# Optimization experiments

Measured on AMD Instinct MI355X. Metric: run time of the kernel, lower is better.

The kernel has to match this reference:

```python
import jax, jax.numpy as jnp
import numpy as np

B, C, H, W = 8, 64, 64, 64


def setup_inputs() -> dict:
    key = jax.random.key(0)
    ks = jax.random.split(key, 8)
    s = 1.0 / np.sqrt(C)  # keep logits in a reasonable range
    return {
        "x": jax.random.normal(ks[0], (B, C, H, W), dtype=jnp.float32),
        "Wf": jax.random.normal(ks[1], (C, C), dtype=jnp.float32) * s,
        "bf": jax.random.normal(ks[2], (C,), dtype=jnp.float32) * s,
        "Wg": jax.random.normal(ks[3], (C, C), dtype=jnp.float32) * s,
        "bg": jax.random.normal(ks[4], (C,), dtype=jnp.float32) * s,
        "Wh": jax.random.normal(ks[5], (C, C), dtype=jnp.float32) * s,
        "bh": jax.random.normal(ks[6], (C,), dtype=jnp.float32) * s,
        "gamma": jax.random.normal(ks[7], (1,), dtype=jnp.float32),
    }


def reference(x, Wf, bf, Wg, bg, Wh, bh, gamma):
    b, c, h, w = x.shape
    n = h * w
    xf = x.reshape(b, c, n)  # [B, C, N]
    # 1x1 convs == per-pixel channel GEMMs
    f = jnp.einsum("oc,bcn->bon", Wf, xf) + bf[None, :, None]  # [B, C, N]
    g = jnp.einsum("oc,bcn->bon", Wg, xf) + bg[None, :, None]
    hh = jnp.einsum("oc,bcn->bon", Wh, xf) + bh[None, :, None]
    # att_in[b, i, j] = f[b, :, i] . g[b, :, j]  (f_x permuted then bmm with g_x)
    att = jax.nn.softmax(jnp.einsum("bci,bcj->bij", f, g), axis=-1)  # [B, N, N]
    # torch.bmm(h_x, attention): out[b, c, j] = sum_i h[b, c, i] * att[b, i, j]
    out = jnp.einsum("bci,bij->bcj", hh, att).reshape(b, c, h, w)
    return gamma[0] * out + x
```

## Files before the change

kernel.cpp:

```cpp
#include <hip/hip_runtime.h>

#define BB 8
#define CC 64
#define NN 4096
#define JCH 8
#define LOG2E 1.4426950408889634f

typedef float f32x4  __attribute__((ext_vector_type(4)));
typedef float f32x16 __attribute__((ext_vector_type(16)));
typedef _Float16 half8_t __attribute__((ext_vector_type(8)));
typedef int int4v __attribute__((ext_vector_type(4)));
typedef unsigned uint2v __attribute__((ext_vector_type(2)));


__global__ __launch_bounds__(384, 6) void qkv_kernel(
    const float* __restrict__ x,
    const float* __restrict__ Wf, const float* __restrict__ bf,
    const float* __restrict__ Wg, const float* __restrict__ bg,
    const float* __restrict__ Wh, const float* __restrict__ bh,
    _Float16* __restrict__ fT, _Float16* __restrict__ gT,
    _Float16* __restrict__ hT)
{
    __shared__ float xbuf[64][36];

    const int tid  = threadIdx.x;
    const int lane = tid & 63;
    const int wv   = tid >> 6;
    const int l31  = lane & 31;
    const int q5   = lane >> 5;
    const int z    = wv >> 1;
    const int ot   = wv & 1;
    const int n0   = blockIdx.x * 32;
    const int b    = blockIdx.y;

    if (tid < 256) {
        const int row = tid >> 2;
        const int px4 = (tid & 3) * 8;
        const float* src = x + (size_t)(b * CC + row) * NN + n0 + px4;
        *(f32x4*)&xbuf[row][px4]     = *(const f32x4*)(src);
        *(f32x4*)&xbuf[row][px4 + 4] = *(const f32x4*)(src + 4);
    }
    __syncthreads();

    half8_t xf[4];
#pragma unroll
    for (int kc = 0; kc < 4; ++kc) {
        const int kb = kc * 16 + q5 * 8;
        int4v p;
#pragma unroll
        for (int h2 = 0; h2 < 4; ++h2) {
            p[h2] = __builtin_bit_cast(int, __builtin_amdgcn_cvt_pkrtz(
                xbuf[kb + h2 * 2][l31], xbuf[kb + h2 * 2 + 1][l31]));
        }
        xf[kc] = __builtin_bit_cast(half8_t, p);
    }

    const float* W    = (z == 0) ? Wf : ((z == 1) ? Wg : Wh);
    const float* bias = (z == 0) ? bf : ((z == 1) ? bg : bh);

    half8_t wf[4];
    {
        const float* wrow = W + (size_t)(ot * 32 + l31) * CC;
#pragma unroll
        for (int kc = 0; kc < 4; ++kc) {
            const f32x4 w0 = *(const f32x4*)(wrow + kc * 16 + q5 * 8);
            const f32x4 w1 = *(const f32x4*)(wrow + kc * 16 + q5 * 8 + 4);
            int4v p;
            p[0] = __builtin_bit_cast(int, __builtin_amdgcn_cvt_pkrtz(w0[0], w0[1]));
            p[1] = __builtin_bit_cast(int, __builtin_amdgcn_cvt_pkrtz(w0[2], w0[3]));
            p[2] = __builtin_bit_cast(int, __builtin_amdgcn_cvt_pkrtz(w1[0], w1[1]));
            p[3] = __builtin_bit_cast(int, __builtin_amdgcn_cvt_pkrtz(w1[2], w1[3]));
            wf[kc] = __builtin_bit_cast(half8_t, p);
        }
    }

    if (z < 2) {
        f32x16 acc = {};
#pragma unroll
        for (int kc = 0; kc < 4; ++kc)
            acc = __builtin_amdgcn_mfma_f32_32x32x16_f16(xf[kc], wf[kc], acc, 0, 0, 0);
        _Float16* dstT = (z == 0) ? fT : gT;
        const float scale = (z == 0) ? LOG2E : 1.0f;
        const float bv = bias[ot * 32 + l31];
#pragma unroll
        for (int r = 0; r < 16; ++r) {
            const int prow = (r & 3) + 8 * (r >> 2) + 4 * q5;
            dstT[(size_t)(b * NN + n0 + prow) * CC + ot * 32 + l31] =
                (_Float16)((acc[r] + bv) * scale);
        }
    } else {
        f32x16 acc = {};
#pragma unroll
        for (int kc = 0; kc < 4; ++kc)
            acc = __builtin_amdgcn_mfma_f32_32x32x16_f16(wf[kc], xf[kc], acc, 0, 0, 0);
        _Float16* hbase = hT + ((size_t)(b * (NN / 32) + blockIdx.x) * CC) * 32;
#pragma unroll
        for (int rb = 0; rb < 4; ++rb) {
            const f32x4 b4 = *(const f32x4*)(bias + ot * 32 + rb * 8 + q5 * 4);
#pragma unroll
            for (int k = 0; k < 4; ++k) {
                const int c = ot * 32 + rb * 8 + q5 * 4 + k;
                hbase[(size_t)c * 32 + l31] = (_Float16)(acc[rb * 4 + k] + b4[k]);
            }
        }
    }
}

__global__ __launch_bounds__(256, 4) void stats_kernel(
    const _Float16* __restrict__ fT, const _Float16* __restrict__ gT,
    float* __restrict__ lpart)
{
    __shared__ _Float16 gbuf[2][64][72];

    const int lane = threadIdx.x & 63;
    const int wv   = threadIdx.x >> 6;
    const int b    = blockIdx.y;
    const int jc   = blockIdx.z;
    const int i0   = blockIdx.x * 128 + wv * 32;
    const int l31  = lane & 31;
    const int q5   = lane >> 5;

    half8_t a[4];
    const _Float16* fa = fT + (size_t)(b * NN + i0 + l31) * CC + q5 * 8;
#pragma unroll
    for (int kc = 0; kc < 4; ++kc) a[kc] = *(const half8_t*)(fa + kc * 16);

    const _Float16* gchunk = gT + (size_t)(b * NN + jc * (NN / JCH)) * CC;
    const int T = NN / JCH / 64;

    const int srow = wv * 16 + (lane >> 3);
    const int scol = (lane & 7) * 8;

    {
        const half8_t v0 = *(const half8_t*)(gchunk + (size_t)srow * CC + scol);
        const half8_t v1 = *(const half8_t*)(gchunk + (size_t)(srow + 8) * CC + scol);
        *(half8_t*)&gbuf[0][srow][scol] = v0;
        *(half8_t*)&gbuf[0][srow + 8][scol] = v1;
    }
    __syncthreads();

    float l16[16];
#pragma unroll
    for (int r = 0; r < 16; ++r) l16[r] = 0.f;

    for (int t = 0; t < T; ++t) {
        const int buf = t & 1;
        const bool pf = (t + 1 < T);
        half8_t p0, p1;
        if (pf) {
            const _Float16* src = gchunk + (size_t)((t + 1) * 64 + srow) * CC + scol;
            p0 = *(const half8_t*)(src);
            p1 = *(const half8_t*)(src + 8 * CC);
        }
#pragma unroll
        for (int js = 0; js < 2; ++js) {
            const _Float16* grow = &gbuf[buf][js * 32 + l31][0] + q5 * 8;
            f32x16 s = {};
#pragma unroll
            for (int kc = 0; kc < 4; ++kc) {
                const half8_t bfr = *(const half8_t*)(grow + kc * 16);
                s = __builtin_amdgcn_mfma_f32_32x32x16_f16(a[kc], bfr, s, 0, 0, 0);
            }
#pragma unroll
            for (int r = 0; r < 16; ++r) l16[r] += __builtin_exp2f(s[r]);
        }
        if (pf) {
            *(half8_t*)&gbuf[buf ^ 1][srow][scol] = p0;
            *(half8_t*)&gbuf[buf ^ 1][srow + 8][scol] = p1;
        }
        __syncthreads();
    }

#pragma unroll
    for (int r = 0; r < 16; ++r) {
#pragma unroll
        for (int off = 1; off < 32; off <<= 1)
            l16[r] += __shfl_xor(l16[r], off);
    }

    if (l31 == 0) {
        float* lp = lpart + (size_t)jc * BB * NN + b * NN + i0;
#pragma unroll
        for (int rb = 0; rb < 4; ++rb) {
            f32x4 v;
#pragma unroll
            for (int k = 0; k < 4; ++k) v[k] = l16[rb * 4 + k];
            *(f32x4*)(lp + rb * 8 + q5 * 4) = v;
        }
    }
}

template <int NICT>
__global__ __launch_bounds__(256, 2) void attn_kernel(
    const _Float16* __restrict__ fT, const _Float16* __restrict__ gT,
    const _Float16* __restrict__ hT, const float* __restrict__ lpart,
    _Float16* __restrict__ pout)
{
    constexpr int ichunk = NN / NICT;
    __shared__ _Float16 fbuf[2][2][64][72];
    __shared__ _Float16 hbuf[2][2][64][72];
    __shared__ float nbbuf[ichunk];

    const int lane = threadIdx.x & 63;
    const int wv   = threadIdx.x >> 6;
    const int b    = blockIdx.y;
    const int ic   = blockIdx.z;
    const int l31  = lane & 31;
    const int q5   = lane >> 5;
    const int jbase = blockIdx.x * 256 + wv * 64;

    const int ibase  = ic * ichunk;
    const int tid    = threadIdx.x;

    if (tid * 4 < ichunk) {
        const float* lp0 = lpart + b * NN + ibase + tid * 4;
        f32x4 sum = *(const f32x4*)(lp0);
#pragma unroll
        for (int jc = 1; jc < JCH; ++jc) {
            const f32x4 v = *(const f32x4*)(lp0 + (size_t)jc * BB * NN);
#pragma unroll
            for (int k = 0; k < 4; ++k) sum[k] += v[k];
        }
        f32x4 nb4;
#pragma unroll
        for (int k = 0; k < 4; ++k) nb4[k] = -__builtin_log2f(sum[k]);
        *(f32x4*)&nbbuf[tid * 4] = nb4;
    }

    half8_t bg[2][4];
#pragma unroll
    for (int jt = 0; jt < 2; ++jt) {
        const _Float16* grow = gT + (size_t)(b * NN + jbase + jt * 32 + l31) * CC + q5 * 8;
#pragma unroll
        for (int kc = 0; kc < 4; ++kc) bg[jt][kc] = *(const half8_t*)(grow + kc * 16);
    }

    f32x16 acc[2][2] = {};

    const _Float16* fchunk = fT + ((size_t)b * NN + ibase) * CC;
    const _Float16* hchunk = hT + ((size_t)(b * (NN / 32) + ibase / 32) * CC) * 32;
    const int TP = (ichunk / 64) / 2;

    const int frow_s = tid >> 2;
    const int fcol_s = (tid & 3) * 16;
    const int hrow_s = tid >> 2;
    const int hcol_s = (tid & 3) * 8;

#pragma unroll
    for (int th = 0; th < 2; ++th) {
        const _Float16* fsrc = fchunk + (size_t)(th * 64 + frow_s) * CC + fcol_s;
        const _Float16* hsrc = hchunk + (size_t)th * 4096 + tid * 8;
        *(half8_t*)&fbuf[0][th][frow_s][fcol_s]     = *(const half8_t*)(fsrc);
        *(half8_t*)&fbuf[0][th][frow_s][fcol_s + 8] = *(const half8_t*)(fsrc + 8);
        *(half8_t*)&hbuf[0][th][hrow_s][hcol_s]      = *(const half8_t*)(hsrc);
        *(half8_t*)&hbuf[0][th][hrow_s][32 + hcol_s] = *(const half8_t*)(hsrc + 2048);
    }
    __syncthreads();

    for (int tp = 0; tp < TP; ++tp) {
        const int buf = tp & 1;
        const bool pf = (tp + 1 < TP);
        half8_t pf0[2], pf1[2], ph0[2], ph1[2];
        if (pf) {
#pragma unroll
            for (int th = 0; th < 2; ++th) {
                const int t = (tp + 1) * 2 + th;
                const _Float16* fsrc = fchunk + (size_t)(t * 64 + frow_s) * CC + fcol_s;
                const _Float16* hsrc = hchunk + (size_t)t * 4096 + tid * 8;
                pf0[th] = *(const half8_t*)(fsrc);
                pf1[th] = *(const half8_t*)(fsrc + 8);
                ph0[th] = *(const half8_t*)(hsrc);
                ph1[th] = *(const half8_t*)(hsrc + 2048);
            }
        }

#pragma unroll
        for (int th = 0; th < 2; ++th) {
            const int t = tp * 2 + th;

            f32x16 s[2][2];
#pragma unroll
            for (int ih = 0; ih < 2; ++ih) {
                f32x16 si;
#pragma unroll
                for (int rb = 0; rb < 4; ++rb) {
                    const f32x4 n4 = *(const f32x4*)&nbbuf[t * 64 + ih * 32 + rb * 8 + q5 * 4];
#pragma unroll
                    for (int k = 0; k < 4; ++k) si[rb * 4 + k] = n4[k];
                }
                s[ih][0] = si;
                s[ih][1] = si;
            }
            __builtin_amdgcn_s_setprio(1);
#pragma unroll
            for (int ih = 0; ih < 2; ++ih) {
                const _Float16* frow = &fbuf[buf][th][ih * 32 + l31][0] + q5 * 8;
#pragma unroll
                for (int kc = 0; kc < 4; ++kc) {
                    const half8_t af = *(const half8_t*)(frow + kc * 16);
                    s[ih][0] = __builtin_amdgcn_mfma_f32_32x32x16_f16(af, bg[0][kc], s[ih][0], 0, 0, 0);
                    s[ih][1] = __builtin_amdgcn_mfma_f32_32x32x16_f16(af, bg[1][kc], s[ih][1], 0, 0, 0);
                }
            }
            __builtin_amdgcn_s_setprio(0);

            half8_t B[2][2][2];
#pragma unroll
            for (int ih = 0; ih < 2; ++ih) {
#pragma unroll
                for (int jt = 0; jt < 2; ++jt) {
                    const f32x16& sv = s[ih][jt];
                    int e[8];
#pragma unroll
                    for (int r8 = 0; r8 < 8; ++r8) {
                        e[r8] = __builtin_bit_cast(int, __builtin_amdgcn_cvt_pkrtz(
                            __builtin_exp2f(sv[r8 * 2]), __builtin_exp2f(sv[r8 * 2 + 1])));
                    }
                    int4v b0, b1;
#if __has_builtin(__builtin_amdgcn_permlane32_swap)
                    const uint2v p02 = __builtin_amdgcn_permlane32_swap(
                        (unsigned)e[0], (unsigned)e[2], false, false);
                    const uint2v p13 = __builtin_amdgcn_permlane32_swap(
                        (unsigned)e[1], (unsigned)e[3], false, false);
                    const uint2v p46 = __builtin_amdgcn_permlane32_swap(
                        (unsigned)e[4], (unsigned)e[6], false, false);
                    const uint2v p57 = __builtin_amdgcn_permlane32_swap(
                        (unsigned)e[5], (unsigned)e[7], false, false);
                    b0[0] = (int)p02[0]; b0[1] = (int)p13[0];
                    b0[2] = (int)p02[1]; b0[3] = (int)p13[1];
                    b1[0] = (int)p46[0]; b1[1] = (int)p57[0];
                    b1[2] = (int)p46[1]; b1[3] = (int)p57[1];
#else
                    const int sA = q5 ? e[0] : e[2];
                    const int sB = q5 ? e[1] : e[3];
                    const int sC = q5 ? e[4] : e[6];
                    const int sD = q5 ? e[5] : e[7];
                    const int rA = __shfl_xor(sA, 32, 64);
                    const int rB = __shfl_xor(sB, 32, 64);
                    const int rC = __shfl_xor(sC, 32, 64);
                    const int rD = __shfl_xor(sD, 32, 64);
                    b0[0] = q5 ? rA   : e[0];
                    b0[1] = q5 ? rB   : e[1];
                    b0[2] = q5 ? e[2] : rA;
                    b0[3] = q5 ? e[3] : rB;
                    b1[0] = q5 ? rC   : e[4];
                    b1[1] = q5 ? rD   : e[5];
                    b1[2] = q5 ? e[6] : rC;
                    b1[3] = q5 ? e[7] : rD;
#endif
                    B[ih][jt][0] = __builtin_bit_cast(half8_t, b0);
                    B[ih][jt][1] = __builtin_bit_cast(half8_t, b1);
                }
            }

            __builtin_amdgcn_s_setprio(1);
#pragma unroll
            for (int ih = 0; ih < 2; ++ih) {
#pragma unroll
                for (int ct = 0; ct < 2; ++ct) {
                    const half8_t ah0 = *(const half8_t*)(&hbuf[buf][th][ct * 32 + l31][0] + ih * 32 + q5 * 8);
                    const half8_t ah1 = *(const half8_t*)(&hbuf[buf][th][ct * 32 + l31][0] + ih * 32 + 16 + q5 * 8);
                    acc[0][ct] = __builtin_amdgcn_mfma_f32_32x32x16_f16(ah0, B[ih][0][0], acc[0][ct], 0, 0, 0);
                    acc[0][ct] = __builtin_amdgcn_mfma_f32_32x32x16_f16(ah1, B[ih][0][1], acc[0][ct], 0, 0, 0);
                    acc[1][ct] = __builtin_amdgcn_mfma_f32_32x32x16_f16(ah0, B[ih][1][0], acc[1][ct], 0, 0, 0);
                    acc[1][ct] = __builtin_amdgcn_mfma_f32_32x32x16_f16(ah1, B[ih][1][1], acc[1][ct], 0, 0, 0);
                }
            }
            __builtin_amdgcn_s_setprio(0);
        }

        if (pf) {
#pragma unroll
            for (int th = 0; th < 2; ++th) {
                *(half8_t*)&fbuf[buf ^ 1][th][frow_s][fcol_s]     = pf0[th];
                *(half8_t*)&fbuf[buf ^ 1][th][frow_s][fcol_s + 8] = pf1[th];
                *(half8_t*)&hbuf[buf ^ 1][th][hrow_s][hcol_s]      = ph0[th];
                *(half8_t*)&hbuf[buf ^ 1][th][hrow_s][32 + hcol_s] = ph1[th];
            }
        }
        __syncthreads();
    }

    _Float16* pb_out = pout + (((size_t)ic * BB + b) * CC) * NN;
#pragma unroll
    for (int jt = 0; jt < 2; ++jt) {
        const int j = jbase + jt * 32 + l31;
#pragma unroll
        for (int ct = 0; ct < 2; ++ct) {
#pragma unroll
            for (int r = 0; r < 16; ++r) {
                const int c = ct * 32 + (r & 3) + 8 * (r >> 2) + 4 * q5;
                pb_out[(size_t)c * NN + j] = (_Float16)acc[jt][ct][r];
            }
        }
    }
}

template <int NICT>
__global__ __launch_bounds__(256) void combine_kernel(
    const float* __restrict__ x, const float* __restrict__ gammap,
    const _Float16* __restrict__ pout, float* __restrict__ out)
{
    const float gam = gammap[0];
    const size_t i8 = ((size_t)blockIdx.x * 256 + threadIdx.x) * 8;
    const size_t TOT = (size_t)BB * CC * NN;

    float s[8] = {0.f, 0.f, 0.f, 0.f, 0.f, 0.f, 0.f, 0.f};
#pragma unroll
    for (int ic = 0; ic < NICT; ++ic) {
        const half8_t p = *(const half8_t*)(pout + ic * TOT + i8);
#pragma unroll
        for (int k = 0; k < 8; ++k) s[k] += (float)p[k];
    }
    const f32x4 x0 = *(const f32x4*)(x + i8);
    const f32x4 x1 = *(const f32x4*)(x + i8 + 4);
    f32x4 o0, o1;
#pragma unroll
    for (int k = 0; k < 4; ++k) { o0[k] = gam * s[k] + x0[k]; o1[k] = gam * s[k + 4] + x1[k]; }
    *(f32x4*)(out + i8) = o0;
    *(f32x4*)(out + i8 + 4) = o1;
}

extern "C" void kernel_launch(void* const* d_in, const int* in_sizes, int n_in,
                              void* d_out, int out_size, void* d_ws, size_t ws_size,
                              hipStream_t stream) {
    const float* x     = (const float*)d_in[0];
    const float* Wf    = (const float*)d_in[1];
    const float* bf    = (const float*)d_in[2];
    const float* Wg    = (const float*)d_in[3];
    const float* bg    = (const float*)d_in[4];
    const float* Wh    = (const float*)d_in[5];
    const float* bh    = (const float*)d_in[6];
    const float* gamma = (const float*)d_in[7];
    float* out = (float*)d_out;

    const size_t TOT = (size_t)BB * CC * NN;
    _Float16* fT   = (_Float16*)d_ws;
    _Float16* gT   = fT + TOT;
    _Float16* hT   = gT + TOT;
    _Float16* pout = hT + TOT;
    float* lpart   = (float*)(pout + (size_t)4 * TOT);

    qkv_kernel<<<dim3(NN / 32, BB), 384, 0, stream>>>(
        x, Wf, bf, Wg, bg, Wh, bh, fT, gT, hT);
    stats_kernel<<<dim3(NN / 128, BB, JCH), 256, 0, stream>>>(fT, gT, lpart);
    attn_kernel<4><<<dim3(NN / 256, BB, 4), 256, 0, stream>>>(fT, gT, hT, lpart, pout);
    combine_kernel<4><<<dim3(TOT / (256 * 8)), 256, 0, stream>>>(x, gamma, pout, out);
}
```

Measured before the change: 167.8 us.

## Fuse split-i combine into attention kernel via last-block atomic counter

Removes the separate combine kernel. Each attention block now signals completion through an agent-scope atomic counter per (batch, j-tile), and the last of the NICT i-chunk blocks sums the fp16 partials, applies gamma and adds the residual. This saves one kernel launch and lets the reduction run on partials that are likely still in cache. In exchange it adds a memset launch, fences, and a serialized tail of work on the last-arriving blocks.

```diff
diff --git a/kernel.cpp b/kernel.cpp
--- a/kernel.cpp
+++ b/kernel.cpp
@@ -194,12 +194,15 @@
 __global__ __launch_bounds__(256, 2) void attn_kernel(
     const _Float16* __restrict__ fT, const _Float16* __restrict__ gT,
     const _Float16* __restrict__ hT, const float* __restrict__ lpart,
-    _Float16* __restrict__ pout)
+    _Float16* __restrict__ pout,
+    const float* __restrict__ xres, const float* __restrict__ gammap,
+    float* __restrict__ outp, unsigned* __restrict__ cnt)
 {
     constexpr int ichunk = NN / NICT;
     __shared__ _Float16 fbuf[2][2][64][72];
     __shared__ _Float16 hbuf[2][2][64][72];
     __shared__ float nbbuf[ichunk];
+    __shared__ unsigned done_cnt;
 
     const int lane = threadIdx.x & 63;
     const int wv   = threadIdx.x >> 6;
@@ -394,31 +397,43 @@
             }
         }
     }
-}
-
-template <int NICT>
-__global__ __launch_bounds__(256) void combine_kernel(
-    const float* __restrict__ x, const float* __restrict__ gammap,
-    const _Float16* __restrict__ pout, float* __restrict__ out)
-{
-    const float gam = gammap[0];
-    const size_t i8 = ((size_t)blockIdx.x * 256 + threadIdx.x) * 8;
-    const size_t TOT = (size_t)BB * CC * NN;
-
-    float s[8] = {0.f, 0.f, 0.f, 0.f, 0.f, 0.f, 0.f, 0.f};
-#pragma unroll
-    for (int ic = 0; ic < NICT; ++ic) {
-        const half8_t p = *(const half8_t*)(pout + ic * TOT + i8);
-#pragma unroll
-        for (int k = 0; k < 8; ++k) s[k] += (float)p[k];
-    }
-    const f32x4 x0 = *(const f32x4*)(x + i8);
-    const f32x4 x1 = *(const f32x4*)(x + i8 + 4);
-    f32x4 o0, o1;
-#pragma unroll
-    for (int k = 0; k < 4; ++k) { o0[k] = gam * s[k] + x0[k]; o1[k] = gam * s[k + 4] + x1[k]; }
-    *(f32x4*)(out + i8) = o0;
-    *(f32x4*)(out + i8 + 4) = o1;
+
+    __threadfence();
+    if (tid == 0) {
+        done_cnt = __hip_atomic_fetch_add(cnt + (b * 16 + blockIdx.x), 1u,
+                       __ATOMIC_ACQ_REL, __HIP_MEMORY_SCOPE_AGENT);
+    }
+    __syncthreads();
+    if (done_cnt == (unsigned)(NICT - 1)) {
+        __threadfence();
+        const float gam = gammap[0];
+        const size_t TOT = (size_t)BB * CC * NN;
+        const int jb0 = blockIdx.x * 256;
+#pragma unroll
+        for (int it = 0; it < 8; ++it) {
+            const int idx = it * 256 + tid;
+            const int c   = idx >> 5;
+            const int j8  = (idx & 31) * 8;
+            const size_t off = ((size_t)b * CC + c) * NN + jb0 + j8;
+            float sacc[8] = {0.f, 0.f, 0.f, 0.f, 0.f, 0.f, 0.f, 0.f};
+#pragma unroll
+            for (int icc = 0; icc < NICT; ++icc) {
+                const half8_t p = *(const half8_t*)(pout + (size_t)icc * TOT + off);
+#pragma unroll
+                for (int k = 0; k < 8; ++k) sacc[k] += (float)p[k];
+            }
+            const f32x4 x0 = *(const f32x4*)(xres + off);
+            const f32x4 x1 = *(const f32x4*)(xres + off + 4);
+            f32x4 o0, o1;
+#pragma unroll
+            for (int k = 0; k < 4; ++k) {
+                o0[k] = gam * sacc[k] + x0[k];
+                o1[k] = gam * sacc[k + 4] + x1[k];
+            }
+            *(f32x4*)(outp + off) = o0;
+            *(f32x4*)(outp + off + 4) = o1;
+        }
+    }
 }
 
 extern "C" void kernel_launch(void* const* d_in, const int* in_sizes, int n_in,
@@ -440,10 +455,12 @@
     _Float16* hT   = gT + TOT;
     _Float16* pout = hT + TOT;
     float* lpart   = (float*)(pout + (size_t)4 * TOT);
-
+    unsigned* cnt  = (unsigned*)(lpart + (size_t)JCH * BB * NN);
+
+    hipMemsetAsync(cnt, 0, 16 * BB * sizeof(unsigned), stream);
     qkv_kernel<<<dim3(NN / 32, BB), 384, 0, stream>>>(
         x, Wf, bf, Wg, bg, Wh, bh, fT, gT, hT);
     stats_kernel<<<dim3(NN / 128, BB, JCH), 256, 0, stream>>>(fT, gT, lpart);
-    attn_kernel<4><<<dim3(NN / 256, BB, 4), 256, 0, stream>>>(fT, gT, hT, lpart, pout);
-    combine_kernel<4><<<dim3(TOT / (256 * 8)), 256, 0, stream>>>(x, gamma, pout, out);
+    attn_kernel<4><<<dim3(NN / 256, BB, 4), 256, 0, stream>>>(
+        fT, gT, hT, lpart, pout, x, gamma, out, cnt);
 }
```

New measurement: 253.9 us. +51.3%, slower.
